# Kernel tuning notes

Hardware: AMD Instinct MI355X
Metric: run time of the kernel (lower is better)

## Reference

```python
import jax, jax.numpy as jnp
import numpy as np

D_MODEL = 512
N_HEADS = 8
D_HEAD = D_MODEL // N_HEADS
D_FF = 2048
L_Q = 22          # forecast_horizon
FACTOR = 5        # prob_sparse_factor
EPS = 1e-5


def positional_encoding(L, d):
    pos = jnp.arange(L, dtype=jnp.float32)[:, None]
    div = jnp.exp(-jnp.arange(0, d, 2, dtype=jnp.float32) * (np.log(10000.0) / d))
    pe = jnp.zeros((L, d), dtype=jnp.float32)
    pe = pe.at[:, 0::2].set(jnp.sin(pos * div))
    pe = pe.at[:, 1::2].set(jnp.cos(pos * div))
    return pe


def layernorm(x, g, b):
    mu = x.mean(-1, keepdims=True)
    var = ((x - mu) ** 2).mean(-1, keepdims=True)
    return (x - mu) * jax.lax.rsqrt(var + EPS) * g + b


def setup_inputs() -> dict:
    key = jax.random.key(0)
    ks = jax.random.split(key, 8)
    s = 0.02
    return {
        "encoder_output": jax.random.normal(ks[0], (32, 4096, D_MODEL), dtype=jnp.float32),
        "Wq": jax.random.normal(ks[1], (D_MODEL, D_MODEL), dtype=jnp.float32) * s,
        "bq": jnp.zeros((D_MODEL,), jnp.float32),
        "Wk": jax.random.normal(ks[2], (D_MODEL, D_MODEL), dtype=jnp.float32) * s,
        "bk": jnp.zeros((D_MODEL,), jnp.float32),
        "Wv": jax.random.normal(ks[3], (D_MODEL, D_MODEL), dtype=jnp.float32) * s,
        "bv": jnp.zeros((D_MODEL,), jnp.float32),
        "Wo": jax.random.normal(ks[4], (D_MODEL, D_MODEL), dtype=jnp.float32) * s,
        "bo": jnp.zeros((D_MODEL,), jnp.float32),
        "conv1_w": jax.random.normal(ks[5], (D_FF, D_MODEL), dtype=jnp.float32) * s,  # Conv1d k=1
        "conv1_b": jnp.zeros((D_FF,), jnp.float32),
        "conv2_w": jax.random.normal(ks[6], (D_MODEL, D_FF), dtype=jnp.float32) * s,
        "conv2_b": jnp.zeros((D_MODEL,), jnp.float32),
        "gamma1": jnp.ones((D_MODEL,), jnp.float32),
        "beta1": jnp.zeros((D_MODEL,), jnp.float32),
        "gamma2": jnp.ones((D_MODEL,), jnp.float32),
        "beta2": jnp.zeros((D_MODEL,), jnp.float32),
        "Wout": jax.random.normal(ks[7], (D_MODEL, 1), dtype=jnp.float32) * s,
        "bout": jnp.zeros((1,), jnp.float32),
    }


def reference(encoder_output, Wq, bq, Wk, bk, Wv, bv, Wo, bo,
              conv1_w, conv1_b, conv2_w, conv2_b,
              gamma1, beta1, gamma2, beta2, Wout, bout):
    B, L_K, _ = encoder_output.shape
    # queries are pure positional encodings of a zero dummy input
    pe = positional_encoding(L_Q, D_MODEL)[None]                      # [1, L_Q, d]
    q = (pe @ Wq + bq).reshape(1, L_Q, N_HEADS, D_HEAD).transpose(0, 2, 1, 3)
    k = (encoder_output @ Wk + bk).reshape(B, L_K, N_HEADS, D_HEAD).transpose(0, 2, 1, 3)
    v = (encoder_output @ Wv + bv).reshape(B, L_K, N_HEADS, D_HEAD).transpose(0, 2, 1, 3)

    # --- deterministic ProbSparse query selection (Informer-style) ---
    sample_k = min(L_K, FACTOR * int(np.ceil(np.log(L_K))))           # 45
    n_top = min(L_Q, FACTOR * int(np.ceil(np.log(L_Q))))              # 20
    k_idx = (jnp.arange(sample_k) * L_K) // sample_k                  # deterministic strided key sample
    k_samp = k[:, :, k_idx]                                           # [B,h,sk,dh]
    qk_s = jnp.einsum('ahqd,bhkd->bhqk', q, k_samp)                   # [B,h,L_Q,sk]
    M = qk_s.max(-1) - qk_s.mean(-1)                                  # sparsity measure [B,h,L_Q]
    _, top_idx = jax.lax.top_k(M, n_top)                              # [B,h,n_top]

    q_b = jnp.broadcast_to(q, (B, N_HEADS, L_Q, D_HEAD))
    q_top = jnp.take_along_axis(q_b, top_idx[..., None], axis=2)      # [B,h,n_top,dh]
    scale = 1.0 / np.sqrt(D_HEAD)
    attn = jax.nn.softmax(jnp.einsum('bhud,bhkd->bhuk', q_top, k) * scale, axis=-1)
    ctx_top = jnp.einsum('bhuk,bhkd->bhud', attn, v)                  # [B,h,n_top,dh]

    # non-selected queries get mean(V) (no causal mask: cross attention)
    ctx = jnp.broadcast_to(v.mean(axis=2, keepdims=True), (B, N_HEADS, L_Q, D_HEAD))
    b_i = jnp.arange(B)[:, None, None]
    h_i = jnp.arange(N_HEADS)[None, :, None]
    ctx = ctx.at[b_i, h_i, top_idx].set(ctx_top)

    attn_out = ctx.transpose(0, 2, 1, 3).reshape(B, L_Q, D_MODEL) @ Wo + bo

    # eval-mode dropout is identity -> norm1(attn + dropout(attn)) == norm1(2*attn)
    x = layernorm(attn_out + attn_out, gamma1, beta1)
    ff = jax.nn.relu(x @ conv1_w.T + conv1_b)                          # conv1d k=1 == pointwise linear
    ff = ff @ conv2_w.T + conv2_b
    y = layernorm(x + ff, gamma2, beta2)                               # [B,L_Q,d]
    forecasts = (y @ Wout + bout).squeeze(-1)                          # [B,L_Q]
    return forecasts, y
```

## Files before the change

### kernel.cpp

```cpp
#include <hip/hip_runtime.h>
#include <math.h>

#define B_ 32
#define LK 4096
#define C_ 512
#define H_ 8
#define DH 64
#define U_ 22
#define HU 176
#define HUP 192
#define SK 45
#define NTOP 20
#define DFF 2048
#define EPSF 1e-5f

typedef unsigned short u16;
typedef __attribute__((ext_vector_type(8))) short short8;
typedef __attribute__((ext_vector_type(4))) short short4v;
typedef __attribute__((ext_vector_type(8))) unsigned short ushort8;
typedef __attribute__((ext_vector_type(4))) unsigned short ushort4v;
typedef __attribute__((ext_vector_type(4))) float f32x4;

__device__ __forceinline__ u16 f2b(float f){
  union{float f;unsigned u;} v; v.f=f;
  unsigned r=(v.u + 0x7FFFu + ((v.u>>16)&1u))>>16;
  return (u16)r;
}
__device__ __forceinline__ float b2f(u16 h){
  union{unsigned u;float f;} v; v.u=((unsigned)h)<<16; return v.f;
}
__device__ __forceinline__ short8 ldfrag(const u16* p){
  short4v lo=*(const short4v*)p;
  short4v hi=*(const short4v*)(p+16);
  short8 r;
  r[0]=lo[0];r[1]=lo[1];r[2]=lo[2];r[3]=lo[3];
  r[4]=hi[0];r[5]=hi[1];r[6]=hi[2];r[7]=hi[3];
  return r;
}
__device__ __forceinline__ float blocksum(float v, float* red){
  for(int off=32;off;off>>=1) v+=__shfl_xor(v,off);
  int w=threadIdx.x>>6, lane=threadIdx.x&63;
  if(lane==0) red[w]=v;
  __syncthreads();
  float r=red[0]+red[1]+red[2]+red[3];
  __syncthreads();
  return r;
}

__global__ void k_prep_q(const float* __restrict__ Wq, const float* __restrict__ bq,
                         float* __restrict__ q){
  __shared__ float pe[C_];
  int u=blockIdx.x, t=threadIdx.x;
  float lg = logf(10000.0f)/(float)C_;
  for(int c=t;c<C_;c+=256){
    int i=c>>1;
    float arg=(float)u*expf(-(float)(2*i)*lg);
    pe[c]=(c&1)?cosf(arg):sinf(arg);
  }
  __syncthreads();
  for(int col=t;col<C_;col+=256){
    float acc=0.f;
    for(int c=0;c<C_;c++) acc+=pe[c]*Wq[c*C_+col];
    q[u*C_+col]=acc+bq[col];
  }
}

__global__ void k_qeff(const float* __restrict__ q, const float* __restrict__ Wk,
                       float* __restrict__ qef, u16* __restrict__ qeb){
  int hu=blockIdx.x, t=threadIdx.x;
  int h=hu/U_, u=hu-h*U_;
  __shared__ float qr[DH];
  bool valid=(hu<HU);
  if(t<DH) qr[t]=valid? q[u*C_+h*DH+t] : 0.f;
  __syncthreads();
  for(int c=t;c<C_;c+=256){
    float acc=0.f;
    if(valid){
      const float* wrow=Wk+(size_t)c*C_+h*DH;
      for(int d=0;d<DH;d++) acc+=qr[d]*wrow[d];
    }
    qef[hu*C_+c]=acc;
    qeb[hu*C_+c]=f2b(acc);
  }
}

__global__ void k_sample(const float* __restrict__ enc, const float* __restrict__ qef,
                         unsigned* __restrict__ selmask){
  int bh=blockIdx.x, t=threadIdx.x;
  int b=bh>>3, h=bh&7;
  __shared__ float es[SK][132];
  __shared__ float qe[U_][132];
  __shared__ float qk[U_][SK+3];
  __shared__ float Mv[U_];
  float acc[4]={0.f,0.f,0.f,0.f};
  for(int c0=0;c0<C_;c0+=128){
    __syncthreads();
    for(int i=t;i<SK*128;i+=256){
      int ks=i>>7, c=i&127;
      int row=(ks*LK)/SK;
      es[ks][c]=enc[((size_t)b*LK+row)*C_+c0+c];
    }
    for(int i=t;i<U_*128;i+=256){
      int u=i>>7, c=i&127;
      qe[u][c]=qef[(h*U_+u)*C_+c0+c];
    }
    __syncthreads();
    for(int dd=0;dd<4;dd++){
      int d=t+dd*256;
      if(d<U_*SK){
        int u=d/SK, ks=d-u*SK;
        float s=0.f;
        for(int c=0;c<128;c++) s+=qe[u][c]*es[ks][c];
        acc[dd]+=s;
      }
    }
  }
  for(int dd=0;dd<4;dd++){
    int d=t+dd*256;
    if(d<U_*SK){ int u=d/SK, ks=d-u*SK; qk[u][ks]=acc[dd]; }
  }
  __syncthreads();
  if(t<U_){
    float mx=-1e30f, sm=0.f;
    for(int ks=0;ks<SK;ks++){ float v=qk[t][ks]; mx=fmaxf(mx,v); sm+=v; }
    Mv[t]=mx-sm/(float)SK;
  }
  __syncthreads();
  if(t<64){
    bool sel=false;
    if(t<U_){
      float m=Mv[t]; int rank=0;
      for(int u2=0;u2<U_;u2++){
        float o=Mv[u2];
        if(o>m || (o==m && u2<t)) rank++;
      }
      sel=(rank<NTOP);
    }
    unsigned long long bal=__ballot(sel);
    if(t==0) selmask[bh]=(unsigned)(bal&0x3FFFFFull);
  }
}

__global__ void k_convert(const float* __restrict__ enc, u16* __restrict__ encb,
                          u16* __restrict__ encT){
  int ct=blockIdx.x, lt=blockIdx.y, b=blockIdx.z, t=threadIdx.x;
  __shared__ __align__(16) u16 tile[64][72];
  int l0=lt*64, c0=ct*64;
  for(int p=0;p<4;p++){
    int lr=p*16+(t>>4);
    int cc=(t&15)*4;
    float4 v=*(const float4*)&enc[((size_t)b*LK+l0+lr)*C_+c0+cc];
    u16 h0=f2b(v.x),h1=f2b(v.y),h2=f2b(v.z),h3=f2b(v.w);
    ushort4v o; o[0]=h0;o[1]=h1;o[2]=h2;o[3]=h3;
    *(ushort4v*)&encb[((size_t)b*LK+l0+lr)*C_+c0+cc]=o;
    tile[cc+0][lr]=h0; tile[cc+1][lr]=h1; tile[cc+2][lr]=h2; tile[cc+3][lr]=h3;
  }
  __syncthreads();
  for(int p=0;p<2;p++){
    int cr=p*32+(t>>3), loff=(t&7)*8;
    ushort8 w=*(const ushort8*)&tile[cr][loff];
    *(ushort8*)&encT[((size_t)b*C_+c0+cr)*LK+l0+loff]=w;
  }
}

__global__ void k_colsum(const u16* __restrict__ encT, float* __restrict__ encsum){
  int b=blockIdx.x;
  int w=threadIdx.x>>6, lane=threadIdx.x&63;
  int c=blockIdx.y*4+w;
  const u16* row=encT+((size_t)b*C_+c)*LK;
  float s=0.f;
  for(int i=0;i<8;i++){
    ushort8 v=*(const ushort8*)&row[(i*64+lane)*8];
    for(int j=0;j<8;j++) s+=b2f(v[j]);
  }
  for(int off=32;off;off>>=1) s+=__shfl_down(s,off);
  if(lane==0) encsum[b*C_+c]=s;
}

__global__ __launch_bounds__(256) void k_scores(const u16* __restrict__ encb,
                                                const u16* __restrict__ qeb,
                                                u16* __restrict__ S){
  int mt=blockIdx.x, nt=blockIdx.y, b=blockIdx.z, t=threadIdx.x;
  __shared__ __align__(16) u16 qa[32][40];
  __shared__ __align__(16) u16 et[256][40];
  int hu0=mt*32, l0=nt*256;
  int w=t>>6, lane=t&63;
  int arow=lane&15, kgrp=(lane>>4)*4;
  f32x4 acc[2][4];
  #pragma unroll
  for(int i=0;i<2;i++)
    #pragma unroll
    for(int j=0;j<4;j++) acc[i][j]=(f32x4){0.f,0.f,0.f,0.f};
  for(int kc=0;kc<C_;kc+=32){
    __syncthreads();
    if(t<128){
      int r=t>>2, off=(t&3)*8;
      *(ushort8*)&qa[r][off]=*(const ushort8*)&qeb[(hu0+r)*C_+kc+off];
    }
    for(int i=t;i<1024;i+=256){
      int l=i>>2, off=(i&3)*8;
      *(ushort8*)&et[l][off]=*(const ushort8*)&encb[((size_t)b*LK+l0+l)*C_+kc+off];
    }
    __syncthreads();
    short8 af0=ldfrag(&qa[arow][kgrp]);
    short8 af1=ldfrag(&qa[16+arow][kgrp]);
    #pragma unroll
    for(int ns=0;ns<4;ns++){
      short8 bf=ldfrag(&et[w*64+ns*16+arow][kgrp]);
      acc[0][ns]=__builtin_amdgcn_mfma_f32_16x16x32_bf16(af0,bf,acc[0][ns],0,0,0);
      acc[1][ns]=__builtin_amdgcn_mfma_f32_16x16x32_bf16(af1,bf,acc[1][ns],0,0,0);
    }
  }
  int dcol=lane&15, drow=(lane>>4)*4;
  #pragma unroll
  for(int ms=0;ms<2;ms++)
    #pragma unroll
    for(int ns=0;ns<4;ns++){
      size_t base=((size_t)b*HUP+hu0+ms*16+drow)*LK + l0 + w*64 + ns*16 + dcol;
      #pragma unroll
      for(int r=0;r<4;r++)
        S[base+(size_t)r*LK]=f2b(acc[ms][ns][r]);
    }
}

__global__ void k_softmax(u16* __restrict__ S){
  int hu=blockIdx.x, b=blockIdx.y, t=threadIdx.x;
  u16* row=S+((size_t)b*HUP+hu)*LK;
  __shared__ float red[8];
  __shared__ float red2[8];
  float v[16];
  ushort8 r0=*(const ushort8*)&row[t*16];
  ushort8 r1=*(const ushort8*)&row[t*16+8];
  #pragma unroll
  for(int j=0;j<8;j++){ v[j]=b2f(r0[j]); v[8+j]=b2f(r1[j]); }
  float mx=-1e30f;
  #pragma unroll
  for(int j=0;j<16;j++) mx=fmaxf(mx,v[j]);
  for(int off=32;off;off>>=1) mx=fmaxf(mx,__shfl_xor(mx,off));
  int w=t>>6, lane=t&63;
  if(lane==0) red[w]=mx;
  __syncthreads();
  mx=fmaxf(fmaxf(red[0],red[1]),fmaxf(red[2],red[3]));
  const float scale=0.125f;
  float sm=0.f;
  #pragma unroll
  for(int j=0;j<16;j++){ v[j]=__expf((v[j]-mx)*scale); sm+=v[j]; }
  for(int off=32;off;off>>=1) sm+=__shfl_xor(sm,off);
  if(lane==0) red2[w]=sm;
  __syncthreads();
  sm=red2[0]+red2[1]+red2[2]+red2[3];
  float inv=1.f/sm;
  ushort8 o0,o1;
  #pragma unroll
  for(int j=0;j<8;j++){ o0[j]=f2b(v[j]*inv); o1[j]=f2b(v[8+j]*inv); }
  *(ushort8*)&row[t*16]=o0;
  *(ushort8*)&row[t*16+8]=o1;
}

__global__ __launch_bounds__(256) void k_pv(const u16* __restrict__ S,
                                            const u16* __restrict__ encT,
                                            float* __restrict__ ctxA){
  int mt=blockIdx.x, nt=blockIdx.y, bz=blockIdx.z, t=threadIdx.x;
  int b=bz>>2, kch=bz&3;
  __shared__ __align__(16) u16 pa[48][72];
  __shared__ __align__(16) u16 et[128][72];
  int hu0=mt*48, c0=nt*128;
  int w=t>>6, lane=t&63;
  int arow=lane&15, kgrp=(lane>>4)*4;
  f32x4 acc[3][2];
  #pragma unroll
  for(int i=0;i<3;i++)
    #pragma unroll
    for(int j=0;j<2;j++) acc[i][j]=(f32x4){0.f,0.f,0.f,0.f};
  int lbase=kch*1024;
  for(int l0=lbase;l0<lbase+1024;l0+=64){
    __syncthreads();
    for(int i=t;i<384;i+=256){
      int r=i>>3, off=(i&7)*8;
      *(ushort8*)&pa[r][off]=*(const ushort8*)&S[((size_t)b*HUP+hu0+r)*LK+l0+off];
    }
    for(int i=t;i<1024;i+=256){
      int r=i>>3, off=(i&7)*8;
      *(ushort8*)&et[r][off]=*(const ushort8*)&encT[((size_t)b*C_+c0+r)*LK+l0+off];
    }
    __syncthreads();
    #pragma unroll
    for(int ks=0;ks<2;ks++){
      short8 af0=ldfrag(&pa[arow][ks*32+kgrp]);
      short8 af1=ldfrag(&pa[16+arow][ks*32+kgrp]);
      short8 af2=ldfrag(&pa[32+arow][ks*32+kgrp]);
      #pragma unroll
      for(int ns=0;ns<2;ns++){
        short8 bf=ldfrag(&et[w*32+ns*16+arow][ks*32+kgrp]);
        acc[0][ns]=__builtin_amdgcn_mfma_f32_16x16x32_bf16(af0,bf,acc[0][ns],0,0,0);
        acc[1][ns]=__builtin_amdgcn_mfma_f32_16x16x32_bf16(af1,bf,acc[1][ns],0,0,0);
        acc[2][ns]=__builtin_amdgcn_mfma_f32_16x16x32_bf16(af2,bf,acc[2][ns],0,0,0);
      }
    }
  }
  int dcol=lane&15, drow=(lane>>4)*4;
  #pragma unroll
  for(int m=0;m<3;m++)
    #pragma unroll
    for(int ns=0;ns<2;ns++)
      #pragma unroll
      for(int r=0;r<4;r++){
        int hu=hu0+m*16+drow+r, c=c0+w*32+ns*16+dcol;
        atomicAdd(&ctxA[((size_t)b*HUP+hu)*C_+c],acc[m][ns][r]);
      }
}

__global__ void k_ctxproj(const float* __restrict__ ctxA, const float* __restrict__ encsum,
                          const unsigned* __restrict__ selmask, const float* __restrict__ Wv,
                          const float* __restrict__ bv, float* __restrict__ ctx){
  int u=blockIdx.x, b=blockIdx.y, t=threadIdx.x;
  __shared__ float R[H_][C_];
  for(int h=0;h<H_;h++){
    bool sel=(selmask[b*H_+h]>>u)&1u;
    const float* src=sel? &ctxA[((size_t)b*HUP+h*U_+u)*C_] : &encsum[b*C_];
    float sc=sel? 1.f : (1.f/(float)LK);
    for(int c=t;c<C_;c+=256) R[h][c]=src[c]*sc;
  }
  __syncthreads();
  for(int hd=t;hd<C_;hd+=256){
    int h=hd>>6;
    float a=0.f;
    for(int c=0;c<C_;c++) a+=R[h][c]*Wv[(size_t)c*C_+hd];
    ctx[((size_t)(b*U_+u))*C_+hd]=a+bv[hd];
  }
}

__global__ void k_wo_ln1(const float* __restrict__ ctx, const float* __restrict__ Wo,
                         const float* __restrict__ bo, const float* __restrict__ g1,
                         const float* __restrict__ be1, float* __restrict__ x,
                         u16* __restrict__ xb){
  int u=blockIdx.x, b=blockIdx.y, t=threadIdx.x;
  __shared__ float row[C_];
  __shared__ float red[8];
  size_t r0=(size_t)(b*U_+u)*C_;
  for(int c=t;c<C_;c+=256) row[c]=ctx[r0+c];
  __syncthreads();
  float a0=0.f,a1=0.f;
  for(int c=0;c<C_;c++){
    float rv=row[c];
    a0+=rv*Wo[(size_t)c*C_+t];
    a1+=rv*Wo[(size_t)c*C_+t+256];
  }
  a0=2.f*(a0+bo[t]); a1=2.f*(a1+bo[t+256]);
  float mu=blocksum(a0+a1,red)*(1.f/(float)C_);
  float d0=a0-mu, d1=a1-mu;
  float var=blocksum(d0*d0+d1*d1,red)*(1.f/(float)C_);
  float rs=rsqrtf(var+EPSF);
  float x0=d0*rs*g1[t]+be1[t];
  float x1=d1*rs*g1[t+256]+be1[t+256];
  x[r0+t]=x0;
  x[r0+t+256]=x1;
  xb[r0+t]=f2b(x0);
  xb[r0+t+256]=f2b(x1);
}

__global__ void k_convw(const float* __restrict__ W1, const float* __restrict__ W2,
                        u16* __restrict__ W1b, u16* __restrict__ W2b){
  size_t i=((size_t)blockIdx.x*256+threadIdx.x)*8;
  const float* src; u16* dst;
  const size_t NW=(size_t)DFF*C_;
  if(i<NW){ src=W1; dst=W1b; } else { src=W2; dst=W2b; i-=NW; }
  float4 a=*(const float4*)&src[i];
  float4 b=*(const float4*)&src[i+4];
  ushort8 o;
  o[0]=f2b(a.x);o[1]=f2b(a.y);o[2]=f2b(a.z);o[3]=f2b(a.w);
  o[4]=f2b(b.x);o[5]=f2b(b.y);o[6]=f2b(b.z);o[7]=f2b(b.w);
  *(ushort8*)&dst[i]=o;
}

__global__ __launch_bounds__(256) void k_ff1m(const u16* __restrict__ xb,
                                              const u16* __restrict__ W1b,
                                              const float* __restrict__ b1,
                                              u16* __restrict__ ff1b){
  int mt=blockIdx.x, ntb=blockIdx.y, t=threadIdx.x;
  __shared__ __align__(16) u16 a_lds[32][520];
  __shared__ __align__(16) u16 et[256][40];
  int m0=mt*32, n0=ntb*256;
  for(int i=t;i<32*64;i+=256){
    int r=i>>6, cc=(i&63)*8;
    *(ushort8*)&a_lds[r][cc]=*(const ushort8*)&xb[(size_t)(m0+r)*C_+cc];
  }
  int w=t>>6, lane=t&63;
  int arow=lane&15, kgrp=(lane>>4)*4;
  f32x4 acc[2][4];
  #pragma unroll
  for(int i=0;i<2;i++)
    #pragma unroll
    for(int j=0;j<4;j++) acc[i][j]=(f32x4){0.f,0.f,0.f,0.f};
  for(int kc=0;kc<C_;kc+=32){
    __syncthreads();
    for(int i=t;i<1024;i+=256){
      int n=i>>2, off=(i&3)*8;
      *(ushort8*)&et[n][off]=*(const ushort8*)&W1b[(size_t)(n0+n)*C_+kc+off];
    }
    __syncthreads();
    short8 af0=ldfrag(&a_lds[arow][kc+kgrp]);
    short8 af1=ldfrag(&a_lds[16+arow][kc+kgrp]);
    #pragma unroll
    for(int ns=0;ns<4;ns++){
      short8 bf=ldfrag(&et[w*64+ns*16+arow][kgrp]);
      acc[0][ns]=__builtin_amdgcn_mfma_f32_16x16x32_bf16(af0,bf,acc[0][ns],0,0,0);
      acc[1][ns]=__builtin_amdgcn_mfma_f32_16x16x32_bf16(af1,bf,acc[1][ns],0,0,0);
    }
  }
  int dcol=lane&15, drow=(lane>>4)*4;
  #pragma unroll
  for(int ms=0;ms<2;ms++)
    #pragma unroll
    for(int ns=0;ns<4;ns++){
      int n=n0+w*64+ns*16+dcol;
      float bb=b1[n];
      #pragma unroll
      for(int r=0;r<4;r++){
        int m=m0+ms*16+drow+r;
        float v=acc[ms][ns][r]+bb;
        ff1b[(size_t)m*DFF+n]=f2b(v>0.f?v:0.f);
      }
    }
}

__global__ __launch_bounds__(256) void k_ff2m(const u16* __restrict__ ff1b,
                                              const u16* __restrict__ W2b,
                                              float* __restrict__ out){
  int mt=blockIdx.x, ntb=blockIdx.y, kch=blockIdx.z, t=threadIdx.x;
  __shared__ __align__(16) u16 a_lds[32][520];
  __shared__ __align__(16) u16 et[256][40];
  int m0=mt*32, n0=ntb*256, k0=kch*512;
  for(int i=t;i<32*64;i+=256){
    int r=i>>6, cc=(i&63)*8;
    *(ushort8*)&a_lds[r][cc]=*(const ushort8*)&ff1b[(size_t)(m0+r)*DFF+k0+cc];
  }
  int w=t>>6, lane=t&63;
  int arow=lane&15, kgrp=(lane>>4)*4;
  f32x4 acc[2][4];
  #pragma unroll
  for(int i=0;i<2;i++)
    #pragma unroll
    for(int j=0;j<4;j++) acc[i][j]=(f32x4){0.f,0.f,0.f,0.f};
  for(int kc=0;kc<512;kc+=32){
    __syncthreads();
    for(int i=t;i<1024;i+=256){
      int n=i>>2, off=(i&3)*8;
      *(ushort8*)&et[n][off]=*(const ushort8*)&W2b[(size_t)(n0+n)*DFF+k0+kc+off];
    }
    __syncthreads();
    short8 af0=ldfrag(&a_lds[arow][kc+kgrp]);
    short8 af1=ldfrag(&a_lds[16+arow][kc+kgrp]);
    #pragma unroll
    for(int ns=0;ns<4;ns++){
      short8 bf=ldfrag(&et[w*64+ns*16+arow][kgrp]);
      acc[0][ns]=__builtin_amdgcn_mfma_f32_16x16x32_bf16(af0,bf,acc[0][ns],0,0,0);
      acc[1][ns]=__builtin_amdgcn_mfma_f32_16x16x32_bf16(af1,bf,acc[1][ns],0,0,0);
    }
  }
  int dcol=lane&15, drow=(lane>>4)*4;
  #pragma unroll
  for(int ms=0;ms<2;ms++)
    #pragma unroll
    for(int ns=0;ns<4;ns++){
      int n=n0+w*64+ns*16+dcol;
      #pragma unroll
      for(int r=0;r<4;r++){
        int m=m0+ms*16+drow+r;
        atomicAdd(&out[(size_t)m*C_+n],acc[ms][ns][r]);
      }
    }
}

__global__ void k_ln2(const float* __restrict__ x, const float* __restrict__ ff2,
                      const float* __restrict__ b2, const float* __restrict__ g2,
                      const float* __restrict__ be2, const float* __restrict__ Wout,
                      const float* __restrict__ bout, float* __restrict__ dout){
  int u=blockIdx.x, b=blockIdx.y, t=threadIdx.x;
  __shared__ float red[8];
  size_t r0=(size_t)(b*U_+u)*C_;
  float s0=x[r0+t]+ff2[r0+t]+b2[t];
  float s1=x[r0+t+256]+ff2[r0+t+256]+b2[t+256];
  float mu=blocksum(s0+s1,red)*(1.f/(float)C_);
  float d0=s0-mu, d1=s1-mu;
  float var=blocksum(d0*d0+d1*d1,red)*(1.f/(float)C_);
  float rs=rsqrtf(var+EPSF);
  float y0=d0*rs*g2[t]+be2[t];
  float y1=d1*rs*g2[t+256]+be2[t+256];
  float* Y=dout+B_*U_;
  Y[r0+t]=y0;
  Y[r0+t+256]=y1;
  float f=blocksum(y0*Wout[t]+y1*Wout[t+256],red);
  if(t==0) dout[b*U_+u]=f+bout[0];
}

extern "C" void kernel_launch(void* const* d_in, const int* in_sizes, int n_in,
                              void* d_out, int out_size, void* d_ws, size_t ws_size,
                              hipStream_t stream){
  (void)in_sizes;(void)n_in;(void)out_size;(void)ws_size;
  const float* enc =(const float*)d_in[0];
  const float* Wq  =(const float*)d_in[1];
  const float* bq  =(const float*)d_in[2];
  const float* Wk  =(const float*)d_in[3];
  const float* Wv  =(const float*)d_in[5];
  const float* bv  =(const float*)d_in[6];
  const float* Wo  =(const float*)d_in[7];
  const float* bo  =(const float*)d_in[8];
  const float* W1  =(const float*)d_in[9];
  const float* b1  =(const float*)d_in[10];
  const float* W2  =(const float*)d_in[11];
  const float* b2  =(const float*)d_in[12];
  const float* g1  =(const float*)d_in[13];
  const float* be1 =(const float*)d_in[14];
  const float* g2  =(const float*)d_in[15];
  const float* be2 =(const float*)d_in[16];
  const float* Wout=(const float*)d_in[17];
  const float* bout=(const float*)d_in[18];

  char* ws=(char*)d_ws;
  float*    q      =(float*)   (ws+0);
  float*    qef    =(float*)   (ws+45056);
  u16*      qeb    =(u16*)     (ws+438272);
  unsigned* selmask=(unsigned*)(ws+634880);
  float*    encsum =(float*)   (ws+635904);
  u16*      encb   =(u16*)     (ws+701440);
  u16*      encT   =(u16*)     (ws+134919168);
  u16*      S      =(u16*)     (ws+269136896);
  float*    ctxA   =(float*)   (ws+701440);
  float*    ctx    =(float*)   (ws+13284352);
  float*    x      =(float*)   (ws+14726144);
  u16*      ff1b   =(u16*)     (ws+16167936);
  float*    ff2    =(float*)   (ws+21935104);
  u16*      W1b    =(u16*)     (ws+23376896);
  u16*      W2b    =(u16*)     (ws+25474048);
  u16*      xb     =(u16*)     (ws+27571200);

  hipLaunchKernelGGL(k_prep_q, dim3(22),      dim3(256),0,stream, Wq,bq,q);
  hipLaunchKernelGGL(k_qeff,   dim3(192),     dim3(256),0,stream, q,Wk,qef,qeb);
  hipLaunchKernelGGL(k_sample, dim3(256),     dim3(256),0,stream, enc,qef,selmask);
  hipLaunchKernelGGL(k_convert,dim3(8,64,32), dim3(256),0,stream, enc,encb,encT);
  hipLaunchKernelGGL(k_colsum, dim3(32,128),  dim3(256),0,stream, encT,encsum);
  hipLaunchKernelGGL(k_scores, dim3(6,16,32), dim3(256),0,stream, encb,qeb,S);
  hipLaunchKernelGGL(k_softmax,dim3(192,32),  dim3(256),0,stream, S);
  hipMemsetAsync(ctxA,0,12582912,stream);
  hipLaunchKernelGGL(k_pv,     dim3(4,4,128), dim3(256),0,stream, S,encT,ctxA);
  hipLaunchKernelGGL(k_ctxproj,dim3(22,32),   dim3(256),0,stream, ctxA,encsum,selmask,Wv,bv,ctx);
  hipLaunchKernelGGL(k_convw,  dim3(1024),    dim3(256),0,stream, W1,W2,W1b,W2b);
  hipLaunchKernelGGL(k_wo_ln1, dim3(22,32),   dim3(256),0,stream, ctx,Wo,bo,g1,be1,x,xb);
  hipLaunchKernelGGL(k_ff1m,   dim3(22,8),    dim3(256),0,stream, xb,W1b,b1,ff1b);
  hipMemsetAsync(ff2,0,1441792,stream);
  hipLaunchKernelGGL(k_ff2m,   dim3(22,2,4),  dim3(256),0,stream, ff1b,W2b,ff2);
  hipLaunchKernelGGL(k_ln2,    dim3(22,32),   dim3(256),0,stream, x,ff2,b2,g2,be2,Wout,bout,(float*)d_out);
}
```

Baseline: 1.054 ms.

## Retile score GEMM over all query rows and remap PV blocks per XCD

The score kernel now has each block cover all 192 query-head rows against a 128-key tile. Previously each block handled 32 rows against 256 keys, so every encoder tile was reloaded six times across M tiles; now it is read once per batch. Each wave holds 24 accumulator tiles, which raises register pressure and may lower occupancy. The PV kernel uses a flattened 1D grid with an XCD-aware index remap so that the blocks sharing an encoder tile land on the same chiplet's L2.

```diff
diff --git a/kernel.cpp b/kernel.cpp
--- a/kernel.cpp
+++ b/kernel.cpp
@@ -180,46 +180,47 @@
 __global__ __launch_bounds__(256) void k_scores(const u16* __restrict__ encb,
                                                 const u16* __restrict__ qeb,
                                                 u16* __restrict__ S){
-  int mt=blockIdx.x, nt=blockIdx.y, b=blockIdx.z, t=threadIdx.x;
-  __shared__ __align__(16) u16 qa[32][40];
-  __shared__ __align__(16) u16 et[256][40];
-  int hu0=mt*32, l0=nt*256;
+  int nt=blockIdx.x, b=blockIdx.y, t=threadIdx.x;
+  __shared__ __align__(16) u16 qa[HUP][40];
+  __shared__ __align__(16) u16 et[128][40];
+  int l0=nt*128;
   int w=t>>6, lane=t&63;
   int arow=lane&15, kgrp=(lane>>4)*4;
-  f32x4 acc[2][4];
-  #pragma unroll
-  for(int i=0;i<2;i++)
-    #pragma unroll
-    for(int j=0;j<4;j++) acc[i][j]=(f32x4){0.f,0.f,0.f,0.f};
+  f32x4 acc[12][2];
+  #pragma unroll
+  for(int i=0;i<12;i++){
+    acc[i][0]=(f32x4){0.f,0.f,0.f,0.f};
+    acc[i][1]=(f32x4){0.f,0.f,0.f,0.f};
+  }
   for(int kc=0;kc<C_;kc+=32){
     __syncthreads();
-    if(t<128){
-      int r=t>>2, off=(t&3)*8;
-      *(ushort8*)&qa[r][off]=*(const ushort8*)&qeb[(hu0+r)*C_+kc+off];
-    }
-    for(int i=t;i<1024;i+=256){
+    for(int i=t;i<768;i+=256){
+      int r=i>>2, off=(i&3)*8;
+      *(ushort8*)&qa[r][off]=*(const ushort8*)&qeb[(size_t)r*C_+kc+off];
+    }
+    for(int i=t;i<512;i+=256){
       int l=i>>2, off=(i&3)*8;
       *(ushort8*)&et[l][off]=*(const ushort8*)&encb[((size_t)b*LK+l0+l)*C_+kc+off];
     }
     __syncthreads();
-    short8 af0=ldfrag(&qa[arow][kgrp]);
-    short8 af1=ldfrag(&qa[16+arow][kgrp]);
-    #pragma unroll
-    for(int ns=0;ns<4;ns++){
-      short8 bf=ldfrag(&et[w*64+ns*16+arow][kgrp]);
-      acc[0][ns]=__builtin_amdgcn_mfma_f32_16x16x32_bf16(af0,bf,acc[0][ns],0,0,0);
-      acc[1][ns]=__builtin_amdgcn_mfma_f32_16x16x32_bf16(af1,bf,acc[1][ns],0,0,0);
+    short8 bf0=ldfrag(&et[w*32+arow][kgrp]);
+    short8 bf1=ldfrag(&et[w*32+16+arow][kgrp]);
+    #pragma unroll
+    for(int m=0;m<12;m++){
+      short8 af=ldfrag(&qa[m*16+arow][kgrp]);
+      acc[m][0]=__builtin_amdgcn_mfma_f32_16x16x32_bf16(af,bf0,acc[m][0],0,0,0);
+      acc[m][1]=__builtin_amdgcn_mfma_f32_16x16x32_bf16(af,bf1,acc[m][1],0,0,0);
     }
   }
   int dcol=lane&15, drow=(lane>>4)*4;
   #pragma unroll
-  for(int ms=0;ms<2;ms++)
-    #pragma unroll
-    for(int ns=0;ns<4;ns++){
-      size_t base=((size_t)b*HUP+hu0+ms*16+drow)*LK + l0 + w*64 + ns*16 + dcol;
+  for(int m=0;m<12;m++)
+    #pragma unroll
+    for(int ns=0;ns<2;ns++){
+      size_t base=((size_t)b*HUP+m*16+drow)*LK + l0 + w*32 + ns*16 + dcol;
       #pragma unroll
       for(int r=0;r<4;r++)
-        S[base+(size_t)r*LK]=f2b(acc[ms][ns][r]);
+        S[base+(size_t)r*LK]=f2b(acc[m][ns][r]);
     }
 }
 
@@ -260,7 +261,10 @@
 __global__ __launch_bounds__(256) void k_pv(const u16* __restrict__ S,
                                             const u16* __restrict__ encT,
                                             float* __restrict__ ctxA){
-  int mt=blockIdx.x, nt=blockIdx.y, bz=blockIdx.z, t=threadIdx.x;
+  int f=blockIdx.x, t=threadIdx.x;
+  int xcd=f&7, s=f>>3;
+  int mt=s&3, g=(s>>2)*8+xcd;
+  int nt=g>>7, bz=g&127;
   int b=bz>>2, kch=bz&3;
   __shared__ __align__(16) u16 pa[48][72];
   __shared__ __align__(16) u16 et[128][72];
@@ -540,10 +544,10 @@
   hipLaunchKernelGGL(k_sample, dim3(256),     dim3(256),0,stream, enc,qef,selmask);
   hipLaunchKernelGGL(k_convert,dim3(8,64,32), dim3(256),0,stream, enc,encb,encT);
   hipLaunchKernelGGL(k_colsum, dim3(32,128),  dim3(256),0,stream, encT,encsum);
-  hipLaunchKernelGGL(k_scores, dim3(6,16,32), dim3(256),0,stream, encb,qeb,S);
+  hipLaunchKernelGGL(k_scores, dim3(32,32),   dim3(256),0,stream, encb,qeb,S);
   hipLaunchKernelGGL(k_softmax,dim3(192,32),  dim3(256),0,stream, S);
   hipMemsetAsync(ctxA,0,12582912,stream);
-  hipLaunchKernelGGL(k_pv,     dim3(4,4,128), dim3(256),0,stream, S,encT,ctxA);
+  hipLaunchKernelGGL(k_pv,     dim3(2048),    dim3(256),0,stream, S,encT,ctxA);
   hipLaunchKernelGGL(k_ctxproj,dim3(22,32),   dim3(256),0,stream, ctxA,encsum,selmask,Wv,bv,ctx);
   hipLaunchKernelGGL(k_convw,  dim3(1024),    dim3(256),0,stream, W1,W2,W1b,W2b);
   hipLaunchKernelGGL(k_wo_ln1, dim3(22,32),   dim3(256),0,stream, ctx,Wo,bo,g1,be1,x,xb);
```

Result: faster. 924.8 us (-12.2%).
